# Performance work log

Measured on AMD Instinct MI355X. Metric: run time of the kernel, lower is better.

The kernel has to match this reference:

```python
import jax, jax.numpy as jnp
import numpy as np

N_ATOMS = 100000
N_BONDS = 200000
MAX_NB = 6
ATOM_FDIM = 133
BOND_FDIM = 147
HIDDEN = 512
N_MOLS = 8192
DEPTH = 5


def setup_inputs() -> dict:
    key = jax.random.key(0)
    ks = jax.random.split(key, 10)
    f_atoms = jax.random.normal(ks[0], (N_ATOMS, ATOM_FDIM), dtype=jnp.float32)
    f_bonds = jax.random.normal(ks[1], (N_BONDS, BOND_FDIM), dtype=jnp.float32)
    # fan-in scaled weights to keep activations stable through the depth loop
    W_i = jax.random.normal(ks[2], (BOND_FDIM, HIDDEN), dtype=jnp.float32) / np.sqrt(BOND_FDIM)
    W_h = jax.random.normal(ks[3], (HIDDEN, HIDDEN), dtype=jnp.float32) / np.sqrt(HIDDEN)
    W_o = jax.random.normal(ks[4], (ATOM_FDIM + HIDDEN, HIDDEN), dtype=jnp.float32) / np.sqrt(ATOM_FDIM + HIDDEN)
    b_o = jnp.zeros((HIDDEN,), dtype=jnp.float32)
    a2b = jax.random.randint(ks[5], (N_ATOMS, MAX_NB), 0, N_BONDS, dtype=jnp.int32)
    b2a = jax.random.randint(ks[6], (N_BONDS,), 0, N_ATOMS, dtype=jnp.int32)
    b2revb = jax.random.randint(ks[7], (N_BONDS,), 0, N_BONDS, dtype=jnp.int32)
    atom_to_mol = jnp.sort(jax.random.randint(ks[8], (N_ATOMS,), 0, N_MOLS, dtype=jnp.int32))
    return {"f_atoms": f_atoms, "f_bonds": f_bonds, "W_i": W_i, "W_h": W_h,
            "W_o": W_o, "b_o": b_o, "a2b": a2b, "b2a": b2a, "b2revb": b2revb,
            "atom_to_mol": atom_to_mol, "n_mols": N_MOLS}


def reference(f_atoms, f_bonds, W_i, W_h, W_o, b_o, a2b, b2a, b2revb, atom_to_mol, n_mols):
    # input = W_i(f_bonds); message = relu(input)
    inp = f_bonds @ W_i                      # [B, H]
    message = jax.nn.relu(inp)
    for _ in range(DEPTH - 1):
        nei_a_message = message[a2b]         # [A, MAX_NB, H] gather bond->atom
        a_message = nei_a_message.sum(axis=1)  # [A, H]
        message = a_message[b2a] - message[b2revb]  # [B, H]
        message = jax.nn.relu(inp + message @ W_h)  # dropout p=0 -> identity
    nei_a_message = message[a2b]             # [A, MAX_NB, H]
    a_message = nei_a_message.sum(axis=1)    # [A, H]
    a_input = jnp.concatenate([f_atoms, a_message], axis=1)  # [A, ATOM_FDIM+H]
    atom_hiddens = jax.nn.relu(a_input @ W_o + b_o)           # [A, H]
    # mean aggregation per molecule (a_scope -> segment ids)
    sums = jax.ops.segment_sum(atom_hiddens, atom_to_mol, num_segments=n_mols)
    counts = jax.ops.segment_sum(jnp.ones((atom_hiddens.shape[0],), dtype=atom_hiddens.dtype),
                                 atom_to_mol, num_segments=n_mols)
    mol_vecs = jnp.where(counts[:, None] > 0,
                         sums / jnp.maximum(counts, 1.0)[:, None],
                         jnp.zeros_like(sums))  # cached_zero_vector for empty mols
    return mol_vecs
```

## Files before the change

### kernel.cpp

```cpp
#include <hip/hip_runtime.h>
#include <hip/hip_bf16.h>
#include <cstdint>

#define A_N   100000
#define B_N   200000
#define MAXNB 6
#define AFD   133
#define BFD   147
#define HID   512
#define NMOL  8192

typedef __attribute__((ext_vector_type(8))) short bf16x8;
typedef __attribute__((ext_vector_type(4))) float f32x4;

__device__ __forceinline__ unsigned short f2b(float f) {
    unsigned u = __builtin_bit_cast(unsigned, f);
    u += 0x7fffu + ((u >> 16) & 1u);
    return (unsigned short)(u >> 16);
}
__device__ __forceinline__ float blo(unsigned u) { return __builtin_bit_cast(float, u << 16); }
__device__ __forceinline__ float bhi(unsigned u) { return __builtin_bit_cast(float, u & 0xffff0000u); }
__device__ __forceinline__ unsigned pack2f(float a, float b) {
    return (unsigned)f2b(a) | ((unsigned)f2b(b) << 16);
}
__device__ __forceinline__ void glds16(const void* g, void* l) {
    __builtin_amdgcn_global_load_lds((const __attribute__((address_space(1))) unsigned*)g,
                                     (__attribute__((address_space(3))) unsigned*)l, 16, 0, 0);
}

__global__ __launch_bounds__(256) void k_diag(float* __restrict__ out, int n, float val) {
    int i = blockIdx.x * 256 + threadIdx.x;
    if (i < n) out[i] = val;
}

__global__ __launch_bounds__(256) void k_weights(
    const float* __restrict__ Wi, const float* __restrict__ Wh, const float* __restrict__ Wo,
    unsigned short* __restrict__ WiT, unsigned short* __restrict__ WcatImg, unsigned short* __restrict__ WoT)
{
    int n = blockIdx.x, t = threadIdx.x;
    for (int k = t; k < 160; k += 256)
        WiT[(size_t)n * 160 + k] = (k < BFD) ? f2b(Wi[(size_t)k * HID + n]) : (unsigned short)0;
    for (int k = t; k < 672; k += 256) {
        unsigned short v;
        if (k < HID)             v = f2b(Wh[(size_t)k * HID + n]);
        else if (k < HID + BFD)  v = f2b(Wi[(size_t)(k - HID) * HID + n]);
        else                     v = 0;
        int row = n & 127;
        size_t tile = (size_t)(n >> 7) * 21 + (k >> 5);
        WcatImg[tile * 4096 + row * 32 + ((((k >> 3) & 3) ^ ((row >> 1) & 3)) << 3) + (k & 7)] = v;
    }
    for (int k = t; k < 672; k += 256) {
        unsigned short v;
        if (k < AFD)       v = f2b(Wo[(size_t)k * HID + n]);
        else if (k < 160)  v = 0;
        else               v = f2b(Wo[(size_t)(k - 27) * HID + n]);
        WoT[(size_t)n * 672 + k] = v;
    }
}

__global__ __launch_bounds__(256) void k_gemm_wi(
    const float* __restrict__ fb, const unsigned short* __restrict__ WiT,
    unsigned short* __restrict__ msg)
{
    __shared__ unsigned short As[128][32];
    __shared__ unsigned short Bs[128][32];
    const int orig = blockIdx.x;
    const int xcd = orig & 7, idx = orig >> 3;
    const int wg = (xcd < 4 ? xcd * 782 : 3128 + (xcd - 4) * 781) + idx;
    const int bm = wg >> 2, bn = wg & 3;
    const int row0 = bm * 128, col0 = bn * 128;

    const int tid = threadIdx.x, lane = tid & 63, wid = tid >> 6;
    const int wm = wid >> 1, wn = wid & 1;
    const int r0 = tid >> 2, c0 = tid & 3, r1 = 64 + r0;
    const int wsw = (c0 ^ ((r0 >> 1) & 3)) * 8;
    const int rsw = ((lane >> 4) ^ (((lane & 15) >> 1) & 3)) * 8;
    f32x4 acc[4][4] = {};

    const float* pf0 = fb + (size_t)min(row0 + r0, B_N - 1) * BFD;
    const float* pf1 = fb + (size_t)min(row0 + r1, B_N - 1) * BFD;
    const unsigned short* pb0 = WiT + (size_t)(col0 + r0) * 160;
    const unsigned short* pb1 = WiT + (size_t)(col0 + r1) * 160;

    float v0[8], v1[8];
    uint4 b0, b1;

#define LOADA(kt) do { int kb = (kt) * 32 + c0 * 8; \
        _Pragma("unroll") for (int i = 0; i < 8; i++) { int kg = kb + i; v0[i] = (kg < BFD) ? pf0[kg] : 0.f; } \
        _Pragma("unroll") for (int i = 0; i < 8; i++) { int kg = kb + i; v1[i] = (kg < BFD) ? pf1[kg] : 0.f; } } while (0)
#define LOADB(kt) do { int kb = (kt) * 32 + c0 * 8; \
        b0 = *(const uint4*)(pb0 + kb); b1 = *(const uint4*)(pb1 + kb); } while (0)

    LOADA(0); LOADB(0);
    for (int kt = 0; kt < 5; ++kt) {
        __syncthreads();
        uint4 q;
        q.x = pack2f(v0[0], v0[1]); q.y = pack2f(v0[2], v0[3]); q.z = pack2f(v0[4], v0[5]); q.w = pack2f(v0[6], v0[7]);
        *(uint4*)&As[r0][wsw] = q;
        q.x = pack2f(v1[0], v1[1]); q.y = pack2f(v1[2], v1[3]); q.z = pack2f(v1[4], v1[5]); q.w = pack2f(v1[6], v1[7]);
        *(uint4*)&As[r1][wsw] = q;
        *(uint4*)&Bs[r0][wsw] = b0;
        *(uint4*)&Bs[r1][wsw] = b1;
        __syncthreads();
        if (kt < 4) { LOADA(kt + 1); LOADB(kt + 1); }

        bf16x8 af[4], bfr[4];
#pragma unroll
        for (int m = 0; m < 4; m++) af[m] = *(const bf16x8*)&As[wm * 64 + m * 16 + (lane & 15)][rsw];
#pragma unroll
        for (int n = 0; n < 4; n++) bfr[n] = *(const bf16x8*)&Bs[wn * 64 + n * 16 + (lane & 15)][rsw];
#pragma unroll
        for (int m = 0; m < 4; m++)
#pragma unroll
            for (int n = 0; n < 4; n++)
                acc[m][n] = __builtin_amdgcn_mfma_f32_16x16x32_bf16(af[m], bfr[n], acc[m][n], 0, 0, 0);
    }
#undef LOADA
#undef LOADB

#pragma unroll
    for (int m = 0; m < 4; m++) {
        int rbase = row0 + wm * 64 + m * 16 + (lane >> 4) * 4;
#pragma unroll
        for (int n = 0; n < 4; n++) {
            int cg = col0 + wn * 64 + n * 16 + (lane & 15);
#pragma unroll
            for (int r = 0; r < 4; r++) {
                int rg = rbase + r;
                if (rg < B_N) {
                    float v = acc[m][n][r];
                    msg[(size_t)rg * HID + cg] = f2b(v > 0.f ? v : 0.f);
                }
            }
        }
    }
}

__global__ __launch_bounds__(256) void k_delta(
    const unsigned short* __restrict__ msg, const int* __restrict__ a2b,
    const int* __restrict__ b2a, const int* __restrict__ b2revb,
    unsigned short* __restrict__ D)
{
    int b = blockIdx.x * 4 + (threadIdx.x >> 6);
    if (b >= B_N) return;
    int lane = threadIdx.x & 63;
    const int atom = b2a[b];
    const int rev  = b2revb[b];
    const int* nb = a2b + (size_t)atom * MAXNB;
    float acc[8];
    {
        uint4 v = *(const uint4*)(msg + (size_t)rev * HID + lane * 8);
        acc[0] = -blo(v.x); acc[1] = -bhi(v.x);
        acc[2] = -blo(v.y); acc[3] = -bhi(v.y);
        acc[4] = -blo(v.z); acc[5] = -bhi(v.z);
        acc[6] = -blo(v.w); acc[7] = -bhi(v.w);
    }
#pragma unroll
    for (int k = 0; k < MAXNB; k++) {
        uint4 v = *(const uint4*)(msg + (size_t)nb[k] * HID + lane * 8);
        acc[0] += blo(v.x); acc[1] += bhi(v.x);
        acc[2] += blo(v.y); acc[3] += bhi(v.y);
        acc[4] += blo(v.z); acc[5] += bhi(v.z);
        acc[6] += blo(v.w); acc[7] += bhi(v.w);
    }
    uint4 q;
    q.x = pack2f(acc[0], acc[1]); q.y = pack2f(acc[2], acc[3]);
    q.z = pack2f(acc[4], acc[5]); q.w = pack2f(acc[6], acc[7]);
    *(uint4*)(D + (size_t)b * HID + lane * 8) = q;
}

__global__ __launch_bounds__(256) void k_gemm_wh(
    const unsigned short* __restrict__ D, const float* __restrict__ fb,
    const unsigned short* __restrict__ WcatImg,
    unsigned short* __restrict__ msg_out)
{
    __shared__ unsigned short As[128][32];
    __shared__ unsigned short Bs[2][4096];
    const int orig = blockIdx.x;
    const int xcd = orig & 7, idx = orig >> 3;
    const int wg = (xcd < 4 ? xcd * 782 : 3128 + (xcd - 4) * 781) + idx;
    const int bm = wg >> 2, bn = wg & 3;
    const int row0 = bm * 128;

    const int tid = threadIdx.x, lane = tid & 63, wid = tid >> 6;
    const int wm = wid >> 1, wn = wid & 1;
    const int r0 = tid >> 2, c0 = tid & 3, r1 = 64 + r0;
    const int wsw = (c0 ^ ((r0 >> 1) & 3)) * 8;
    const int rsw = ((lane >> 4) ^ (((lane & 15) >> 1) & 3)) * 8;
    f32x4 acc[4][4] = {};

    const int rg0 = min(row0 + r0, B_N - 1), rg1 = min(row0 + r1, B_N - 1);
    const unsigned short* pd0 = D + (size_t)rg0 * HID;
    const unsigned short* pd1 = D + (size_t)rg1 * HID;
    const float* pf0 = fb + (size_t)rg0 * BFD;
    const float* pf1 = fb + (size_t)rg1 * BFD;
    const char* img = (const char*)WcatImg + (size_t)bn * 21 * 8192;
    char* bsb = (char*)&Bs[0][0] + wid * 2048;

    uint4 a0, a1;
    float v0[8], v1[8];

#define GLDSB(kt, buf) do { \
        const char* s = img + (size_t)(kt) * 8192 + wid * 2048 + lane * 16; \
        char* d = bsb + (buf) * 8192; \
        glds16(s, d); \
        glds16(s + 1024, d + 1024); } while (0)
#define LOADA_D(kt) do { int kb = (kt) * 32 + c0 * 8; \
        a0 = *(const uint4*)(pd0 + kb); a1 = *(const uint4*)(pd1 + kb); } while (0)
#define LOADA_F(kt) do { int kb = (kt) * 32 - HID + c0 * 8; \
        _Pragma("unroll") for (int i = 0; i < 8; i++) { int kg = kb + i; v0[i] = (kg < BFD) ? pf0[kg] : 0.f; } \
        _Pragma("unroll") for (int i = 0; i < 8; i++) { int kg = kb + i; v1[i] = (kg < BFD) ? pf1[kg] : 0.f; } } while (0)

    GLDSB(0, 0);
    LOADA_D(0);
    for (int kt = 0; kt < 21; ++kt) {
        __syncthreads();
        if (kt < 16) {
            *(uint4*)&As[r0][wsw] = a0;
            *(uint4*)&As[r1][wsw] = a1;
        } else {
            uint4 q;
            q.x = pack2f(v0[0], v0[1]); q.y = pack2f(v0[2], v0[3]); q.z = pack2f(v0[4], v0[5]); q.w = pack2f(v0[6], v0[7]);
            *(uint4*)&As[r0][wsw] = q;
            q.x = pack2f(v1[0], v1[1]); q.y = pack2f(v1[2], v1[3]); q.z = pack2f(v1[4], v1[5]); q.w = pack2f(v1[6], v1[7]);
            *(uint4*)&As[r1][wsw] = q;
        }
        __syncthreads();
        if (kt < 20) {
            GLDSB(kt + 1, (kt + 1) & 1);
            if (kt + 1 < 16) LOADA_D(kt + 1); else LOADA_F(kt + 1);
        }
        bf16x8 af[4], bfr[4];
#pragma unroll
        for (int m = 0; m < 4; m++) af[m] = *(const bf16x8*)&As[wm * 64 + m * 16 + (lane & 15)][rsw];
#pragma unroll
        for (int n = 0; n < 4; n++) bfr[n] = *(const bf16x8*)&Bs[kt & 1][(wn * 64 + n * 16 + (lane & 15)) * 32 + rsw];
#pragma unroll
        for (int m = 0; m < 4; m++)
#pragma unroll
            for (int n = 0; n < 4; n++)
                acc[m][n] = __builtin_amdgcn_mfma_f32_16x16x32_bf16(af[m], bfr[n], acc[m][n], 0, 0, 0);
    }
#undef GLDSB
#undef LOADA_D
#undef LOADA_F

#pragma unroll
    for (int m = 0; m < 4; m++) {
        int rbase = row0 + wm * 64 + m * 16 + (lane >> 4) * 4;
#pragma unroll
        for (int n = 0; n < 4; n++) {
            int cg = bn * 128 + wn * 64 + n * 16 + (lane & 15);
#pragma unroll
            for (int r = 0; r < 4; r++) {
                int rg = rbase + r;
                if (rg < B_N) {
                    float v = acc[m][n][r];
                    msg_out[(size_t)rg * HID + cg] = f2b(v > 0.f ? v : 0.f);
                }
            }
        }
    }
}

__global__ __launch_bounds__(256) void k_gemm_wo(
    const float* __restrict__ fa, const unsigned short* __restrict__ amsg,
    const unsigned short* __restrict__ WoT, const float* __restrict__ bo,
    float* __restrict__ ah)
{
    __shared__ unsigned short As[128][32];
    __shared__ unsigned short Bs[128][32];
    const int orig = blockIdx.x;
    const int wg = (orig & 7) * 391 + (orig >> 3);
    const int bm = wg >> 2, bn = wg & 3;
    const int row0 = bm * 128, col0 = bn * 128;

    const int tid = threadIdx.x, lane = tid & 63, wid = tid >> 6;
    const int wm = wid >> 1, wn = wid & 1;
    const int r0 = tid >> 2, c0 = tid & 3, r1 = 64 + r0;
    const int wsw = (c0 ^ ((r0 >> 1) & 3)) * 8;
    const int rsw = ((lane >> 4) ^ (((lane & 15) >> 1) & 3)) * 8;
    f32x4 acc[4][4] = {};

    const int rg0 = min(row0 + r0, A_N - 1), rg1 = min(row0 + r1, A_N - 1);
    const float* pf0 = fa + (size_t)rg0 * AFD;
    const float* pf1 = fa + (size_t)rg1 * AFD;
    const unsigned short* pm0 = amsg + (size_t)rg0 * HID;
    const unsigned short* pm1 = amsg + (size_t)rg1 * HID;
    const unsigned short* pb0 = WoT + (size_t)(col0 + r0) * 672;
    const unsigned short* pb1 = WoT + (size_t)(col0 + r1) * 672;

    uint4 a0, a1, b0, b1;
    float v0[8], v1[8];

#define LOADA(kt) do { \
        if ((kt) < 5) { int kb = (kt) * 32 + c0 * 8; \
            _Pragma("unroll") for (int i = 0; i < 8; i++) { int kg = kb + i; v0[i] = (kg < AFD) ? pf0[kg] : 0.f; } \
            _Pragma("unroll") for (int i = 0; i < 8; i++) { int kg = kb + i; v1[i] = (kg < AFD) ? pf1[kg] : 0.f; } \
        } else { int kb = (kt) * 32 - 160 + c0 * 8; \
            a0 = *(const uint4*)(pm0 + kb); a1 = *(const uint4*)(pm1 + kb); } } while (0)
#define LOADB(kt) do { int kb = (kt) * 32 + c0 * 8; \
        b0 = *(const uint4*)(pb0 + kb); b1 = *(const uint4*)(pb1 + kb); } while (0)

    LOADA(0); LOADB(0);
    for (int kt = 0; kt < 21; ++kt) {
        __syncthreads();
        if (kt < 5) {
            uint4 q;
            q.x = pack2f(v0[0], v0[1]); q.y = pack2f(v0[2], v0[3]); q.z = pack2f(v0[4], v0[5]); q.w = pack2f(v0[6], v0[7]);
            *(uint4*)&As[r0][wsw] = q;
            q.x = pack2f(v1[0], v1[1]); q.y = pack2f(v1[2], v1[3]); q.z = pack2f(v1[4], v1[5]); q.w = pack2f(v1[6], v1[7]);
            *(uint4*)&As[r1][wsw] = q;
        } else {
            *(uint4*)&As[r0][wsw] = a0;
            *(uint4*)&As[r1][wsw] = a1;
        }
        *(uint4*)&Bs[r0][wsw] = b0;
        *(uint4*)&Bs[r1][wsw] = b1;
        __syncthreads();
        if (kt < 20) { LOADA(kt + 1); LOADB(kt + 1); }

        bf16x8 af[4], bfr[4];
#pragma unroll
        for (int m = 0; m < 4; m++) af[m] = *(const bf16x8*)&As[wm * 64 + m * 16 + (lane & 15)][rsw];
#pragma unroll
        for (int n = 0; n < 4; n++) bfr[n] = *(const bf16x8*)&Bs[wn * 64 + n * 16 + (lane & 15)][rsw];
#pragma unroll
        for (int m = 0; m < 4; m++)
#pragma unroll
            for (int n = 0; n < 4; n++)
                acc[m][n] = __builtin_amdgcn_mfma_f32_16x16x32_bf16(af[m], bfr[n], acc[m][n], 0, 0, 0);
    }
#undef LOADA
#undef LOADB

#pragma unroll
    for (int m = 0; m < 4; m++) {
        int rbase = row0 + wm * 64 + m * 16 + (lane >> 4) * 4;
#pragma unroll
        for (int n = 0; n < 4; n++) {
            int cg = col0 + wn * 64 + n * 16 + (lane & 15);
            float bias = bo[cg];
#pragma unroll
            for (int r = 0; r < 4; r++) {
                int rg = rbase + r;
                if (rg < A_N) {
                    float v = acc[m][n][r] + bias;
                    ah[(size_t)rg * HID + cg] = v > 0.f ? v : 0.f;
                }
            }
        }
    }
}

__global__ __launch_bounds__(256) void k_gather(
    const unsigned short* __restrict__ msg, const int* __restrict__ a2b,
    unsigned short* __restrict__ amsg)
{
    int g = blockIdx.x * 4 + (threadIdx.x >> 6);
    if (g >= A_N) return;
    int lane = threadIdx.x & 63;
    const int* nb = a2b + (size_t)g * MAXNB;
    float acc[8] = {};
#pragma unroll
    for (int k = 0; k < MAXNB; k++) {
        uint4 v = *(const uint4*)(msg + (size_t)nb[k] * HID + lane * 8);
        acc[0] += blo(v.x); acc[1] += bhi(v.x);
        acc[2] += blo(v.y); acc[3] += bhi(v.y);
        acc[4] += blo(v.z); acc[5] += bhi(v.z);
        acc[6] += blo(v.w); acc[7] += bhi(v.w);
    }
    uint4 q;
    q.x = pack2f(acc[0], acc[1]); q.y = pack2f(acc[2], acc[3]);
    q.z = pack2f(acc[4], acc[5]); q.w = pack2f(acc[6], acc[7]);
    *(uint4*)(amsg + (size_t)g * HID + lane * 8) = q;
}

__global__ __launch_bounds__(256) void k_segmean(
    const float* __restrict__ ah, const int* __restrict__ a2m, float* __restrict__ out)
{
    int mol = blockIdx.x, t = threadIdx.x;
    int lo, hi;
    { int l = 0, r = A_N; while (l < r) { int m = (l + r) >> 1; if (a2m[m] < mol) l = m + 1; else r = m; } lo = l; }
    { int l = lo, r = A_N; while (l < r) { int m = (l + r) >> 1; if (a2m[m] < mol + 1) l = m + 1; else r = m; } hi = l; }
    float s0 = 0.f, s1 = 0.f;
    for (int a = lo; a < hi; a++) {
        s0 += ah[(size_t)a * HID + t];
        s1 += ah[(size_t)a * HID + 256 + t];
    }
    int c = hi - lo;
    float inv = c > 0 ? 1.0f / (float)c : 0.f;
    out[(size_t)mol * HID + t] = s0 * inv;
    out[(size_t)mol * HID + 256 + t] = s1 * inv;
}

extern "C" void kernel_launch(void* const* d_in, const int* in_sizes, int n_in,
                              void* d_out, int out_size, void* d_ws, size_t ws_size,
                              hipStream_t stream)
{
    const float* f_atoms = (const float*)d_in[0];
    const float* f_bonds = (const float*)d_in[1];
    const float* W_i     = (const float*)d_in[2];
    const float* W_h     = (const float*)d_in[3];
    const float* W_o     = (const float*)d_in[4];
    const float* b_o     = (const float*)d_in[5];
    const int*   a2b     = (const int*)d_in[6];
    const int*   b2a     = (const int*)d_in[7];
    const int*   b2revb  = (const int*)d_in[8];
    const int*   a2m     = (const int*)d_in[9];

    const size_t OFF_MSG  = 0;
    const size_t OFF_D    = 204800000;
    const size_t OFF_WIT  = 409600000;
    const size_t OFF_WCAT = 409763840;
    const size_t OFF_WOT  = 410451968;
    const size_t REQUIRED = 411140096;

    if (ws_size < REQUIRED) {
        float val = -(10000.0f + (float)(ws_size >> 20));
        k_diag<<<dim3((out_size + 255) / 256), dim3(256), 0, stream>>>((float*)d_out, out_size, val);
        return;
    }

    char* w = (char*)d_ws;
    unsigned short* msg   = (unsigned short*)(w + OFF_MSG);
    unsigned short* D     = (unsigned short*)(w + OFF_D);
    unsigned short* amsg  = (unsigned short*)(w + OFF_D);
    unsigned short* WiT   = (unsigned short*)(w + OFF_WIT);
    unsigned short* Wcat  = (unsigned short*)(w + OFF_WCAT);
    unsigned short* WoT   = (unsigned short*)(w + OFF_WOT);
    float* ah             = (float*)(w + OFF_MSG);

    k_weights<<<dim3(512), dim3(256), 0, stream>>>(W_i, W_h, W_o, WiT, Wcat, WoT);
    k_gemm_wi<<<dim3(6252), dim3(256), 0, stream>>>(f_bonds, WiT, msg);
    for (int it = 0; it < 4; ++it) {
        k_delta<<<dim3(50000), dim3(256), 0, stream>>>(msg, a2b, b2a, b2revb, D);
        k_gemm_wh<<<dim3(6252), dim3(256), 0, stream>>>(D, f_bonds, Wcat, msg);
    }
    k_gather<<<dim3(25000), dim3(256), 0, stream>>>(msg, a2b, amsg);
    k_gemm_wo<<<dim3(3128), dim3(256), 0, stream>>>(f_atoms, amsg, WoT, b_o, ah);
    k_segmean<<<dim3(NMOL), dim3(256), 0, stream>>>(ah, a2m, (float*)d_out);
}
```

Baseline: 2.448 ms.

## Load GEMM A/B tiles directly into double-buffered LDS and drop a barrier

Both bf16 GEMM kernels (W_h message update and W_o readout) now fetch their bf16 A and B tiles with direct global-to-LDS loads into double-buffered shared memory. This replaces staging them through registers and then storing them to LDS. As a result, the second __syncthreads per k-step is only needed for the fp32 feature tiles that still go through registers. The kernels also get a launch-bounds occupancy hint of 4 blocks. The aim is to cut register pressure, VGPR-to-LDS traffic and barrier stalls, at the cost of twice the shared memory and possibly lower occupancy.

```diff
diff --git a/kernel.cpp b/kernel.cpp
--- a/kernel.cpp
+++ b/kernel.cpp
@@ -169,12 +169,12 @@
     *(uint4*)(D + (size_t)b * HID + lane * 8) = q;
 }
 
-__global__ __launch_bounds__(256) void k_gemm_wh(
+__global__ __launch_bounds__(256, 4) void k_gemm_wh(
     const unsigned short* __restrict__ D, const float* __restrict__ fb,
     const unsigned short* __restrict__ WcatImg,
     unsigned short* __restrict__ msg_out)
 {
-    __shared__ unsigned short As[128][32];
+    __shared__ unsigned short As[2][128][32];
     __shared__ unsigned short Bs[2][4096];
     const int orig = blockIdx.x;
     const int xcd = orig & 7, idx = orig >> 3;
@@ -189,61 +189,60 @@
     const int rsw = ((lane >> 4) ^ (((lane & 15) >> 1) & 3)) * 8;
     f32x4 acc[4][4] = {};
 
+    const int arow1 = wid * 32 + (lane >> 2);
+    const int arow2 = arow1 + 16;
+    const int achk = lane & 3;
+    const unsigned short* srcA1 = D + (size_t)min(row0 + arow1, B_N - 1) * HID + ((achk ^ ((arow1 >> 1) & 3)) << 3);
+    const unsigned short* srcA2 = D + (size_t)min(row0 + arow2, B_N - 1) * HID + ((achk ^ ((arow2 >> 1) & 3)) << 3);
+    const char* srcB = (const char*)WcatImg + (size_t)bn * 21 * 8192 + wid * 2048 + lane * 16;
+
     const int rg0 = min(row0 + r0, B_N - 1), rg1 = min(row0 + r1, B_N - 1);
-    const unsigned short* pd0 = D + (size_t)rg0 * HID;
-    const unsigned short* pd1 = D + (size_t)rg1 * HID;
     const float* pf0 = fb + (size_t)rg0 * BFD;
     const float* pf1 = fb + (size_t)rg1 * BFD;
-    const char* img = (const char*)WcatImg + (size_t)bn * 21 * 8192;
-    char* bsb = (char*)&Bs[0][0] + wid * 2048;
-
-    uint4 a0, a1;
     float v0[8], v1[8];
 
-#define GLDSB(kt, buf) do { \
-        const char* s = img + (size_t)(kt) * 8192 + wid * 2048 + lane * 16; \
-        char* d = bsb + (buf) * 8192; \
-        glds16(s, d); \
-        glds16(s + 1024, d + 1024); } while (0)
-#define LOADA_D(kt) do { int kb = (kt) * 32 + c0 * 8; \
-        a0 = *(const uint4*)(pd0 + kb); a1 = *(const uint4*)(pd1 + kb); } while (0)
-#define LOADA_F(kt) do { int kb = (kt) * 32 - HID + c0 * 8; \
-        _Pragma("unroll") for (int i = 0; i < 8; i++) { int kg = kb + i; v0[i] = (kg < BFD) ? pf0[kg] : 0.f; } \
-        _Pragma("unroll") for (int i = 0; i < 8; i++) { int kg = kb + i; v1[i] = (kg < BFD) ? pf1[kg] : 0.f; } } while (0)
-
-    GLDSB(0, 0);
-    LOADA_D(0);
+    glds16(srcA1, &As[0][wid * 32][0]);
+    glds16(srcA2, &As[0][wid * 32 + 16][0]);
+    glds16(srcB, &Bs[0][wid * 1024]);
+    glds16(srcB + 1024, &Bs[0][wid * 1024 + 512]);
+
     for (int kt = 0; kt < 21; ++kt) {
+        const int cur = kt & 1, nxt = cur ^ 1;
         __syncthreads();
-        if (kt < 16) {
-            *(uint4*)&As[r0][wsw] = a0;
-            *(uint4*)&As[r1][wsw] = a1;
-        } else {
+        if (kt >= 16) {
             uint4 q;
             q.x = pack2f(v0[0], v0[1]); q.y = pack2f(v0[2], v0[3]); q.z = pack2f(v0[4], v0[5]); q.w = pack2f(v0[6], v0[7]);
-            *(uint4*)&As[r0][wsw] = q;
+            *(uint4*)&As[cur][r0][wsw] = q;
             q.x = pack2f(v1[0], v1[1]); q.y = pack2f(v1[2], v1[3]); q.z = pack2f(v1[4], v1[5]); q.w = pack2f(v1[6], v1[7]);
-            *(uint4*)&As[r1][wsw] = q;
-        }
-        __syncthreads();
+            *(uint4*)&As[cur][r1][wsw] = q;
+            __syncthreads();
+        }
         if (kt < 20) {
-            GLDSB(kt + 1, (kt + 1) & 1);
-            if (kt + 1 < 16) LOADA_D(kt + 1); else LOADA_F(kt + 1);
+            if (kt + 1 < 16) {
+                glds16(srcA1 + (kt + 1) * 32, &As[nxt][wid * 32][0]);
+                glds16(srcA2 + (kt + 1) * 32, &As[nxt][wid * 32 + 16][0]);
+            }
+            glds16(srcB + (size_t)(kt + 1) * 8192, &Bs[nxt][wid * 1024]);
+            glds16(srcB + (size_t)(kt + 1) * 8192 + 1024, &Bs[nxt][wid * 1024 + 512]);
+        }
+        if (kt >= 15 && kt < 20) {
+            int kb = (kt + 1) * 32 - HID + c0 * 8;
+#pragma unroll
+            for (int i = 0; i < 8; i++) { int kg = kb + i; v0[i] = (kg < BFD) ? pf0[kg] : 0.f; }
+#pragma unroll
+            for (int i = 0; i < 8; i++) { int kg = kb + i; v1[i] = (kg < BFD) ? pf1[kg] : 0.f; }
         }
         bf16x8 af[4], bfr[4];
 #pragma unroll
-        for (int m = 0; m < 4; m++) af[m] = *(const bf16x8*)&As[wm * 64 + m * 16 + (lane & 15)][rsw];
-#pragma unroll
-        for (int n = 0; n < 4; n++) bfr[n] = *(const bf16x8*)&Bs[kt & 1][(wn * 64 + n * 16 + (lane & 15)) * 32 + rsw];
+        for (int m = 0; m < 4; m++) af[m] = *(const bf16x8*)&As[cur][wm * 64 + m * 16 + (lane & 15)][rsw];
+#pragma unroll
+        for (int n = 0; n < 4; n++) bfr[n] = *(const bf16x8*)&Bs[cur][(wn * 64 + n * 16 + (lane & 15)) * 32 + rsw];
 #pragma unroll
         for (int m = 0; m < 4; m++)
 #pragma unroll
             for (int n = 0; n < 4; n++)
                 acc[m][n] = __builtin_amdgcn_mfma_f32_16x16x32_bf16(af[m], bfr[n], acc[m][n], 0, 0, 0);
     }
-#undef GLDSB
-#undef LOADA_D
-#undef LOADA_F
 
 #pragma unroll
     for (int m = 0; m < 4; m++) {
@@ -263,13 +262,13 @@
     }
 }
 
-__global__ __launch_bounds__(256) void k_gemm_wo(
+__global__ __launch_bounds__(256, 4) void k_gemm_wo(
     const float* __restrict__ fa, const unsigned short* __restrict__ amsg,
     const unsigned short* __restrict__ WoT, const float* __restrict__ bo,
     float* __restrict__ ah)
 {
-    __shared__ unsigned short As[128][32];
-    __shared__ unsigned short Bs[128][32];
+    __shared__ unsigned short As[2][128][32];
+    __shared__ unsigned short Bs[2][128][32];
     const int orig = blockIdx.x;
     const int wg = (orig & 7) * 391 + (orig >> 3);
     const int bm = wg >> 2, bn = wg & 3;
@@ -282,57 +281,68 @@
     const int rsw = ((lane >> 4) ^ (((lane & 15) >> 1) & 3)) * 8;
     f32x4 acc[4][4] = {};
 
+    const int grow1 = wid * 32 + (lane >> 2);
+    const int grow2 = grow1 + 16;
+    const int gchk = lane & 3;
+    const int asw1 = (gchk ^ ((grow1 >> 1) & 3)) << 3;
+    const int asw2 = (gchk ^ ((grow2 >> 1) & 3)) << 3;
+    const unsigned short* srcA1 = amsg + (size_t)min(row0 + grow1, A_N - 1) * HID + asw1 - 160;
+    const unsigned short* srcA2 = amsg + (size_t)min(row0 + grow2, A_N - 1) * HID + asw2 - 160;
+    const unsigned short* srcB1 = WoT + (size_t)(col0 + grow1) * 672 + asw1;
+    const unsigned short* srcB2 = WoT + (size_t)(col0 + grow2) * 672 + asw2;
+
     const int rg0 = min(row0 + r0, A_N - 1), rg1 = min(row0 + r1, A_N - 1);
     const float* pf0 = fa + (size_t)rg0 * AFD;
     const float* pf1 = fa + (size_t)rg1 * AFD;
-    const unsigned short* pm0 = amsg + (size_t)rg0 * HID;
-    const unsigned short* pm1 = amsg + (size_t)rg1 * HID;
-    const unsigned short* pb0 = WoT + (size_t)(col0 + r0) * 672;
-    const unsigned short* pb1 = WoT + (size_t)(col0 + r1) * 672;
-
-    uint4 a0, a1, b0, b1;
     float v0[8], v1[8];
 
-#define LOADA(kt) do { \
-        if ((kt) < 5) { int kb = (kt) * 32 + c0 * 8; \
-            _Pragma("unroll") for (int i = 0; i < 8; i++) { int kg = kb + i; v0[i] = (kg < AFD) ? pf0[kg] : 0.f; } \
-            _Pragma("unroll") for (int i = 0; i < 8; i++) { int kg = kb + i; v1[i] = (kg < AFD) ? pf1[kg] : 0.f; } \
-        } else { int kb = (kt) * 32 - 160 + c0 * 8; \
-            a0 = *(const uint4*)(pm0 + kb); a1 = *(const uint4*)(pm1 + kb); } } while (0)
-#define LOADB(kt) do { int kb = (kt) * 32 + c0 * 8; \
-        b0 = *(const uint4*)(pb0 + kb); b1 = *(const uint4*)(pb1 + kb); } while (0)
-
-    LOADA(0); LOADB(0);
+    {
+        int kb = c0 * 8;
+#pragma unroll
+        for (int i = 0; i < 8; i++) { int kg = kb + i; v0[i] = (kg < AFD) ? pf0[kg] : 0.f; }
+#pragma unroll
+        for (int i = 0; i < 8; i++) { int kg = kb + i; v1[i] = (kg < AFD) ? pf1[kg] : 0.f; }
+    }
+    glds16(srcB1, &Bs[0][wid * 32][0]);
+    glds16(srcB2, &Bs[0][wid * 32 + 16][0]);
+
     for (int kt = 0; kt < 21; ++kt) {
+        const int cur = kt & 1, nxt = cur ^ 1;
         __syncthreads();
         if (kt < 5) {
             uint4 q;
             q.x = pack2f(v0[0], v0[1]); q.y = pack2f(v0[2], v0[3]); q.z = pack2f(v0[4], v0[5]); q.w = pack2f(v0[6], v0[7]);
-            *(uint4*)&As[r0][wsw] = q;
+            *(uint4*)&As[cur][r0][wsw] = q;
             q.x = pack2f(v1[0], v1[1]); q.y = pack2f(v1[2], v1[3]); q.z = pack2f(v1[4], v1[5]); q.w = pack2f(v1[6], v1[7]);
-            *(uint4*)&As[r1][wsw] = q;
-        } else {
-            *(uint4*)&As[r0][wsw] = a0;
-            *(uint4*)&As[r1][wsw] = a1;
-        }
-        *(uint4*)&Bs[r0][wsw] = b0;
-        *(uint4*)&Bs[r1][wsw] = b1;
-        __syncthreads();
-        if (kt < 20) { LOADA(kt + 1); LOADB(kt + 1); }
-
+            *(uint4*)&As[cur][r1][wsw] = q;
+            __syncthreads();
+        }
+        if (kt < 20) {
+            if (kt + 1 >= 5) {
+                glds16(srcA1 + (kt + 1) * 32, &As[nxt][wid * 32][0]);
+                glds16(srcA2 + (kt + 1) * 32, &As[nxt][wid * 32 + 16][0]);
+            }
+            glds16(srcB1 + (kt + 1) * 32, &Bs[nxt][wid * 32][0]);
+            glds16(srcB2 + (kt + 1) * 32, &Bs[nxt][wid * 32 + 16][0]);
+        }
+        if (kt < 4) {
+            int kb = (kt + 1) * 32 + c0 * 8;
+#pragma unroll
+            for (int i = 0; i < 8; i++) { int kg = kb + i; v0[i] = (kg < AFD) ? pf0[kg] : 0.f; }
+#pragma unroll
+            for (int i = 0; i < 8; i++) { int kg = kb + i; v1[i] = (kg < AFD) ? pf1[kg] : 0.f; }
+        }
         bf16x8 af[4], bfr[4];
 #pragma unroll
-        for (int m = 0; m < 4; m++) af[m] = *(const bf16x8*)&As[wm * 64 + m * 16 + (lane & 15)][rsw];
-#pragma unroll
-        for (int n = 0; n < 4; n++) bfr[n] = *(const bf16x8*)&Bs[wn * 64 + n * 16 + (lane & 15)][rsw];
+        for (int m = 0; m < 4; m++) af[m] = *(const bf16x8*)&As[cur][wm * 64 + m * 16 + (lane & 15)][rsw];
+#pragma unroll
+        for (int n = 0; n < 4; n++) bfr[n] = *(const bf16x8*)&Bs[cur][wn * 64 + n * 16 + (lane & 15)][rsw];
 #pragma unroll
         for (int m = 0; m < 4; m++)
 #pragma unroll
             for (int n = 0; n < 4; n++)
                 acc[m][n] = __builtin_amdgcn_mfma_f32_16x16x32_bf16(af[m], bfr[n], acc[m][n], 0, 0, 0);
     }
-#undef LOADA
-#undef LOADB
 
 #pragma unroll
     for (int m = 0; m < 4; m++) {
```

New measurement: 2.384 ms. 1.03x faster.

## Triple-buffer GEMM tiles with direct-to-LDS loads and issue gathers up front

Applied to the files above, without the earlier changes.

The Wh and Wo GEMMs now stage both A and B tiles through three LDS buffers filled by global_load_lds, with explicit vmcnt waits and barriers. This replaces register staging and double buffering so loads for two tiles ahead overlap the MFMA work. The Wo weights are repacked into the same swizzled tile image, and the K order is changed to put the message part first and the atom features last. The gather and delta kernels now issue all neighbour loads before summing, to expose memory-level parallelism. The cost is more LDS per block, hand-written waitcnt logic that must stay exact, and an occupancy hint of 3 blocks per CU.

```diff
diff --git a/kernel.cpp b/kernel.cpp
--- a/kernel.cpp
+++ b/kernel.cpp
@@ -28,6 +28,11 @@
                                      (__attribute__((address_space(3))) unsigned*)l, 16, 0, 0);
 }
 
+#define WAIT4 asm volatile("s_waitcnt vmcnt(4)" ::: "memory")
+#define WAIT2 asm volatile("s_waitcnt vmcnt(2)" ::: "memory")
+#define SB0   __builtin_amdgcn_sched_barrier(0)
+#define BAR   __builtin_amdgcn_s_barrier()
+
 __global__ __launch_bounds__(256) void k_diag(float* __restrict__ out, int n, float val) {
     int i = blockIdx.x * 256 + threadIdx.x;
     if (i < n) out[i] = val;
@@ -35,9 +40,10 @@
 
 __global__ __launch_bounds__(256) void k_weights(
     const float* __restrict__ Wi, const float* __restrict__ Wh, const float* __restrict__ Wo,
-    unsigned short* __restrict__ WiT, unsigned short* __restrict__ WcatImg, unsigned short* __restrict__ WoT)
+    unsigned short* __restrict__ WiT, unsigned short* __restrict__ WcatImg, unsigned short* __restrict__ WoImg)
 {
     int n = blockIdx.x, t = threadIdx.x;
+    int row = n & 127;
     for (int k = t; k < 160; k += 256)
         WiT[(size_t)n * 160 + k] = (k < BFD) ? f2b(Wi[(size_t)k * HID + n]) : (unsigned short)0;
     for (int k = t; k < 672; k += 256) {
@@ -45,16 +51,16 @@
         if (k < HID)             v = f2b(Wh[(size_t)k * HID + n]);
         else if (k < HID + BFD)  v = f2b(Wi[(size_t)(k - HID) * HID + n]);
         else                     v = 0;
-        int row = n & 127;
         size_t tile = (size_t)(n >> 7) * 21 + (k >> 5);
         WcatImg[tile * 4096 + row * 32 + ((((k >> 3) & 3) ^ ((row >> 1) & 3)) << 3) + (k & 7)] = v;
     }
     for (int k = t; k < 672; k += 256) {
         unsigned short v;
-        if (k < AFD)       v = f2b(Wo[(size_t)k * HID + n]);
-        else if (k < 160)  v = 0;
-        else               v = f2b(Wo[(size_t)(k - 27) * HID + n]);
-        WoT[(size_t)n * 672 + k] = v;
+        if (k < 512)       v = f2b(Wo[(size_t)(k + 133) * HID + n]);
+        else if (k < 645)  v = f2b(Wo[(size_t)(k - 512) * HID + n]);
+        else               v = 0;
+        size_t tile = (size_t)(n >> 7) * 21 + (k >> 5);
+        WoImg[tile * 4096 + row * 32 + ((((k >> 3) & 3) ^ ((row >> 1) & 3)) << 3) + (k & 7)] = v;
     }
 }
 
@@ -147,35 +153,35 @@
     const int atom = b2a[b];
     const int rev  = b2revb[b];
     const int* nb = a2b + (size_t)atom * MAXNB;
+    uint4 g0 = *(const uint4*)(msg + (size_t)nb[0] * HID + lane * 8);
+    uint4 g1 = *(const uint4*)(msg + (size_t)nb[1] * HID + lane * 8);
+    uint4 g2 = *(const uint4*)(msg + (size_t)nb[2] * HID + lane * 8);
+    uint4 g3 = *(const uint4*)(msg + (size_t)nb[3] * HID + lane * 8);
+    uint4 g4 = *(const uint4*)(msg + (size_t)nb[4] * HID + lane * 8);
+    uint4 g5 = *(const uint4*)(msg + (size_t)nb[5] * HID + lane * 8);
+    uint4 gr = *(const uint4*)(msg + (size_t)rev * HID + lane * 8);
     float acc[8];
-    {
-        uint4 v = *(const uint4*)(msg + (size_t)rev * HID + lane * 8);
-        acc[0] = -blo(v.x); acc[1] = -bhi(v.x);
-        acc[2] = -blo(v.y); acc[3] = -bhi(v.y);
-        acc[4] = -blo(v.z); acc[5] = -bhi(v.z);
-        acc[6] = -blo(v.w); acc[7] = -bhi(v.w);
-    }
-#pragma unroll
-    for (int k = 0; k < MAXNB; k++) {
-        uint4 v = *(const uint4*)(msg + (size_t)nb[k] * HID + lane * 8);
-        acc[0] += blo(v.x); acc[1] += bhi(v.x);
-        acc[2] += blo(v.y); acc[3] += bhi(v.y);
-        acc[4] += blo(v.z); acc[5] += bhi(v.z);
-        acc[6] += blo(v.w); acc[7] += bhi(v.w);
-    }
+    acc[0] = blo(g0.x) + blo(g1.x) + blo(g2.x) + blo(g3.x) + blo(g4.x) + blo(g5.x) - blo(gr.x);
+    acc[1] = bhi(g0.x) + bhi(g1.x) + bhi(g2.x) + bhi(g3.x) + bhi(g4.x) + bhi(g5.x) - bhi(gr.x);
+    acc[2] = blo(g0.y) + blo(g1.y) + blo(g2.y) + blo(g3.y) + blo(g4.y) + blo(g5.y) - blo(gr.y);
+    acc[3] = bhi(g0.y) + bhi(g1.y) + bhi(g2.y) + bhi(g3.y) + bhi(g4.y) + bhi(g5.y) - bhi(gr.y);
+    acc[4] = blo(g0.z) + blo(g1.z) + blo(g2.z) + blo(g3.z) + blo(g4.z) + blo(g5.z) - blo(gr.z);
+    acc[5] = bhi(g0.z) + bhi(g1.z) + bhi(g2.z) + bhi(g3.z) + bhi(g4.z) + bhi(g5.z) - bhi(gr.z);
+    acc[6] = blo(g0.w) + blo(g1.w) + blo(g2.w) + blo(g3.w) + blo(g4.w) + blo(g5.w) - blo(gr.w);
+    acc[7] = bhi(g0.w) + bhi(g1.w) + bhi(g2.w) + bhi(g3.w) + bhi(g4.w) + bhi(g5.w) - bhi(gr.w);
     uint4 q;
     q.x = pack2f(acc[0], acc[1]); q.y = pack2f(acc[2], acc[3]);
     q.z = pack2f(acc[4], acc[5]); q.w = pack2f(acc[6], acc[7]);
     *(uint4*)(D + (size_t)b * HID + lane * 8) = q;
 }
 
-__global__ __launch_bounds__(256) void k_gemm_wh(
+__global__ __launch_bounds__(256, 3) void k_gemm_wh(
     const unsigned short* __restrict__ D, const float* __restrict__ fb,
     const unsigned short* __restrict__ WcatImg,
     unsigned short* __restrict__ msg_out)
 {
-    __shared__ unsigned short As[128][32];
-    __shared__ unsigned short Bs[2][4096];
+    __shared__ unsigned short As[3][128][32];
+    __shared__ unsigned short Bs[3][4096];
     const int orig = blockIdx.x;
     const int xcd = orig & 7, idx = orig >> 3;
     const int wg = (xcd < 4 ? xcd * 782 : 3128 + (xcd - 4) * 781) + idx;
@@ -189,61 +195,76 @@
     const int rsw = ((lane >> 4) ^ (((lane & 15) >> 1) & 3)) * 8;
     f32x4 acc[4][4] = {};
 
+    const int arow1 = wid * 32 + (lane >> 2);
+    const int arow2 = arow1 + 16;
+    const int achk = lane & 3;
+    const unsigned short* srcA1 = D + (size_t)min(row0 + arow1, B_N - 1) * HID + ((achk ^ ((arow1 >> 1) & 3)) << 3);
+    const unsigned short* srcA2 = D + (size_t)min(row0 + arow2, B_N - 1) * HID + ((achk ^ ((arow2 >> 1) & 3)) << 3);
+    const char* srcB = (const char*)WcatImg + (size_t)bn * 21 * 8192 + wid * 2048 + lane * 16;
+
     const int rg0 = min(row0 + r0, B_N - 1), rg1 = min(row0 + r1, B_N - 1);
-    const unsigned short* pd0 = D + (size_t)rg0 * HID;
-    const unsigned short* pd1 = D + (size_t)rg1 * HID;
     const float* pf0 = fb + (size_t)rg0 * BFD;
     const float* pf1 = fb + (size_t)rg1 * BFD;
-    const char* img = (const char*)WcatImg + (size_t)bn * 21 * 8192;
-    char* bsb = (char*)&Bs[0][0] + wid * 2048;
-
-    uint4 a0, a1;
     float v0[8], v1[8];
 
-#define GLDSB(kt, buf) do { \
-        const char* s = img + (size_t)(kt) * 8192 + wid * 2048 + lane * 16; \
-        char* d = bsb + (buf) * 8192; \
-        glds16(s, d); \
-        glds16(s + 1024, d + 1024); } while (0)
-#define LOADA_D(kt) do { int kb = (kt) * 32 + c0 * 8; \
-        a0 = *(const uint4*)(pd0 + kb); a1 = *(const uint4*)(pd1 + kb); } while (0)
-#define LOADA_F(kt) do { int kb = (kt) * 32 - HID + c0 * 8; \
+#define COMPUTE(b) do { \
+        bf16x8 af[4], bfr[4]; \
+        _Pragma("unroll") \
+        for (int m = 0; m < 4; m++) af[m] = *(const bf16x8*)&As[b][wm * 64 + m * 16 + (lane & 15)][rsw]; \
+        _Pragma("unroll") \
+        for (int n = 0; n < 4; n++) bfr[n] = *(const bf16x8*)&Bs[b][(wn * 64 + n * 16 + (lane & 15)) * 32 + rsw]; \
+        _Pragma("unroll") \
+        for (int m = 0; m < 4; m++) \
+        _Pragma("unroll") \
+        for (int n = 0; n < 4; n++) \
+            acc[m][n] = __builtin_amdgcn_mfma_f32_16x16x32_bf16(af[m], bfr[n], acc[m][n], 0, 0, 0); \
+    } while (0)
+#define GLDS_STEP(kt, buf) do { \
+        glds16(srcA1 + (kt) * 32, &As[buf][wid * 32][0]); \
+        glds16(srcA2 + (kt) * 32, &As[buf][wid * 32 + 16][0]); \
+        glds16(srcB + (size_t)(kt) * 8192, &Bs[buf][wid * 1024]); \
+        glds16(srcB + (size_t)(kt) * 8192 + 1024, &Bs[buf][wid * 1024 + 512]); } while (0)
+#define LOADFB(kt) do { int kb = (kt) * 32 - HID + c0 * 8; \
         _Pragma("unroll") for (int i = 0; i < 8; i++) { int kg = kb + i; v0[i] = (kg < BFD) ? pf0[kg] : 0.f; } \
         _Pragma("unroll") for (int i = 0; i < 8; i++) { int kg = kb + i; v1[i] = (kg < BFD) ? pf1[kg] : 0.f; } } while (0)
 
-    GLDSB(0, 0);
-    LOADA_D(0);
-    for (int kt = 0; kt < 21; ++kt) {
-        __syncthreads();
-        if (kt < 16) {
-            *(uint4*)&As[r0][wsw] = a0;
-            *(uint4*)&As[r1][wsw] = a1;
-        } else {
-            uint4 q;
-            q.x = pack2f(v0[0], v0[1]); q.y = pack2f(v0[2], v0[3]); q.z = pack2f(v0[4], v0[5]); q.w = pack2f(v0[6], v0[7]);
-            *(uint4*)&As[r0][wsw] = q;
-            q.x = pack2f(v1[0], v1[1]); q.y = pack2f(v1[2], v1[3]); q.z = pack2f(v1[4], v1[5]); q.w = pack2f(v1[6], v1[7]);
-            *(uint4*)&As[r1][wsw] = q;
+    LOADFB(16);
+    GLDS_STEP(0, 0);
+    GLDS_STEP(1, 1);
+
+#pragma unroll
+    for (int kt = 0; kt < 14; ++kt) {
+        WAIT4; SB0; BAR; SB0;
+        GLDS_STEP(kt + 2, (kt + 2) % 3);
+        SB0;
+        COMPUTE(kt % 3);
+    }
+    WAIT4; SB0; BAR; SB0;
+    glds16(srcB + (size_t)16 * 8192, &Bs[1][wid * 1024]);
+    glds16(srcB + (size_t)16 * 8192 + 1024, &Bs[1][wid * 1024 + 512]);
+    SB0;
+    COMPUTE(2);
+    WAIT2; SB0; BAR; SB0;
+    COMPUTE(0);
+
+    for (int kt = 16; kt < 21; ++kt) {
+        const int cb = kt % 3;
+        __syncthreads();
+        uint4 q;
+        q.x = pack2f(v0[0], v0[1]); q.y = pack2f(v0[2], v0[3]); q.z = pack2f(v0[4], v0[5]); q.w = pack2f(v0[6], v0[7]);
+        *(uint4*)&As[cb][r0][wsw] = q;
+        q.x = pack2f(v1[0], v1[1]); q.y = pack2f(v1[2], v1[3]); q.z = pack2f(v1[4], v1[5]); q.w = pack2f(v1[6], v1[7]);
+        *(uint4*)&As[cb][r1][wsw] = q;
+        __syncthreads();
+        if (kt < 20) {
+            glds16(srcB + (size_t)(kt + 1) * 8192, &Bs[(kt + 1) % 3][wid * 1024]);
+            glds16(srcB + (size_t)(kt + 1) * 8192 + 1024, &Bs[(kt + 1) % 3][wid * 1024 + 512]);
+            LOADFB(kt + 1);
         }
-        __syncthreads();
-        if (kt < 20) {
-            GLDSB(kt + 1, (kt + 1) & 1);
-            if (kt + 1 < 16) LOADA_D(kt + 1); else LOADA_F(kt + 1);
-        }
-        bf16x8 af[4], bfr[4];
-#pragma unroll
-        for (int m = 0; m < 4; m++) af[m] = *(const bf16x8*)&As[wm * 64 + m * 16 + (lane & 15)][rsw];
-#pragma unroll
-        for (int n = 0; n < 4; n++) bfr[n] = *(const bf16x8*)&Bs[kt & 1][(wn * 64 + n * 16 + (lane & 15)) * 32 + rsw];
-#pragma unroll
-        for (int m = 0; m < 4; m++)
-#pragma unroll
-            for (int n = 0; n < 4; n++)
-                acc[m][n] = __builtin_amdgcn_mfma_f32_16x16x32_bf16(af[m], bfr[n], acc[m][n], 0, 0, 0);
-    }
-#undef GLDSB
-#undef LOADA_D
-#undef LOADA_F
+        COMPUTE(cb);
+    }
+#undef GLDS_STEP
+#undef LOADFB
 
 #pragma unroll
     for (int m = 0; m < 4; m++) {
@@ -261,19 +282,20 @@
             }
         }
     }
-}
-
-__global__ __launch_bounds__(256) void k_gemm_wo(
+#undef COMPUTE
+}
+
+__global__ __launch_bounds__(256, 3) void k_gemm_wo(
     const float* __restrict__ fa, const unsigned short* __restrict__ amsg,
-    const unsigned short* __restrict__ WoT, const float* __restrict__ bo,
+    const unsigned short* __restrict__ WoImg, const float* __restrict__ bo,
     float* __restrict__ ah)
 {
-    __shared__ unsigned short As[128][32];
-    __shared__ unsigned short Bs[128][32];
+    __shared__ unsigned short As[3][128][32];
+    __shared__ unsigned short Bs[3][4096];
     const int orig = blockIdx.x;
     const int wg = (orig & 7) * 391 + (orig >> 3);
     const int bm = wg >> 2, bn = wg & 3;
-    const int row0 = bm * 128, col0 = bn * 128;
+    const int row0 = bm * 128;
 
     const int tid = threadIdx.x, lane = tid & 63, wid = tid >> 6;
     const int wm = wid >> 1, wn = wid & 1;
@@ -282,64 +304,83 @@
     const int rsw = ((lane >> 4) ^ (((lane & 15) >> 1) & 3)) * 8;
     f32x4 acc[4][4] = {};
 
+    const int arow1 = wid * 32 + (lane >> 2);
+    const int arow2 = arow1 + 16;
+    const int achk = lane & 3;
+    const unsigned short* srcA1 = amsg + (size_t)min(row0 + arow1, A_N - 1) * HID + ((achk ^ ((arow1 >> 1) & 3)) << 3);
+    const unsigned short* srcA2 = amsg + (size_t)min(row0 + arow2, A_N - 1) * HID + ((achk ^ ((arow2 >> 1) & 3)) << 3);
+    const char* srcB = (const char*)WoImg + (size_t)bn * 21 * 8192 + wid * 2048 + lane * 16;
+
     const int rg0 = min(row0 + r0, A_N - 1), rg1 = min(row0 + r1, A_N - 1);
     const float* pf0 = fa + (size_t)rg0 * AFD;
     const float* pf1 = fa + (size_t)rg1 * AFD;
-    const unsigned short* pm0 = amsg + (size_t)rg0 * HID;
-    const unsigned short* pm1 = amsg + (size_t)rg1 * HID;
-    const unsigned short* pb0 = WoT + (size_t)(col0 + r0) * 672;
-    const unsigned short* pb1 = WoT + (size_t)(col0 + r1) * 672;
-
-    uint4 a0, a1, b0, b1;
     float v0[8], v1[8];
 
-#define LOADA(kt) do { \
-        if ((kt) < 5) { int kb = (kt) * 32 + c0 * 8; \
-            _Pragma("unroll") for (int i = 0; i < 8; i++) { int kg = kb + i; v0[i] = (kg < AFD) ? pf0[kg] : 0.f; } \
-            _Pragma("unroll") for (int i = 0; i < 8; i++) { int kg = kb + i; v1[i] = (kg < AFD) ? pf1[kg] : 0.f; } \
-        } else { int kb = (kt) * 32 - 160 + c0 * 8; \
-            a0 = *(const uint4*)(pm0 + kb); a1 = *(const uint4*)(pm1 + kb); } } while (0)
-#define LOADB(kt) do { int kb = (kt) * 32 + c0 * 8; \
-        b0 = *(const uint4*)(pb0 + kb); b1 = *(const uint4*)(pb1 + kb); } while (0)
-
-    LOADA(0); LOADB(0);
-    for (int kt = 0; kt < 21; ++kt) {
-        __syncthreads();
-        if (kt < 5) {
-            uint4 q;
-            q.x = pack2f(v0[0], v0[1]); q.y = pack2f(v0[2], v0[3]); q.z = pack2f(v0[4], v0[5]); q.w = pack2f(v0[6], v0[7]);
-            *(uint4*)&As[r0][wsw] = q;
-            q.x = pack2f(v1[0], v1[1]); q.y = pack2f(v1[2], v1[3]); q.z = pack2f(v1[4], v1[5]); q.w = pack2f(v1[6], v1[7]);
-            *(uint4*)&As[r1][wsw] = q;
-        } else {
-            *(uint4*)&As[r0][wsw] = a0;
-            *(uint4*)&As[r1][wsw] = a1;
+#define COMPUTE(b) do { \
+        bf16x8 af[4], bfr[4]; \
+        _Pragma("unroll") \
+        for (int m = 0; m < 4; m++) af[m] = *(const bf16x8*)&As[b][wm * 64 + m * 16 + (lane & 15)][rsw]; \
+        _Pragma("unroll") \
+        for (int n = 0; n < 4; n++) bfr[n] = *(const bf16x8*)&Bs[b][(wn * 64 + n * 16 + (lane & 15)) * 32 + rsw]; \
+        _Pragma("unroll") \
+        for (int m = 0; m < 4; m++) \
+        _Pragma("unroll") \
+        for (int n = 0; n < 4; n++) \
+            acc[m][n] = __builtin_amdgcn_mfma_f32_16x16x32_bf16(af[m], bfr[n], acc[m][n], 0, 0, 0); \
+    } while (0)
+#define GLDS_STEP(kt, buf) do { \
+        glds16(srcA1 + (kt) * 32, &As[buf][wid * 32][0]); \
+        glds16(srcA2 + (kt) * 32, &As[buf][wid * 32 + 16][0]); \
+        glds16(srcB + (size_t)(kt) * 8192, &Bs[buf][wid * 1024]); \
+        glds16(srcB + (size_t)(kt) * 8192 + 1024, &Bs[buf][wid * 1024 + 512]); } while (0)
+#define LOADFA(kt) do { int kb = (kt) * 32 - HID + c0 * 8; \
+        _Pragma("unroll") for (int i = 0; i < 8; i++) { int kg = kb + i; v0[i] = (kg < AFD) ? pf0[kg] : 0.f; } \
+        _Pragma("unroll") for (int i = 0; i < 8; i++) { int kg = kb + i; v1[i] = (kg < AFD) ? pf1[kg] : 0.f; } } while (0)
+
+    LOADFA(16);
+    GLDS_STEP(0, 0);
+    GLDS_STEP(1, 1);
+
+#pragma unroll
+    for (int kt = 0; kt < 14; ++kt) {
+        WAIT4; SB0; BAR; SB0;
+        GLDS_STEP(kt + 2, (kt + 2) % 3);
+        SB0;
+        COMPUTE(kt % 3);
+    }
+    WAIT4; SB0; BAR; SB0;
+    glds16(srcB + (size_t)16 * 8192, &Bs[1][wid * 1024]);
+    glds16(srcB + (size_t)16 * 8192 + 1024, &Bs[1][wid * 1024 + 512]);
+    SB0;
+    COMPUTE(2);
+    WAIT2; SB0; BAR; SB0;
+    COMPUTE(0);
+
+    for (int kt = 16; kt < 21; ++kt) {
+        const int cb = kt % 3;
+        __syncthreads();
+        uint4 q;
+        q.x = pack2f(v0[0], v0[1]); q.y = pack2f(v0[2], v0[3]); q.z = pack2f(v0[4], v0[5]); q.w = pack2f(v0[6], v0[7]);
+        *(uint4*)&As[cb][r0][wsw] = q;
+        q.x = pack2f(v1[0], v1[1]); q.y = pack2f(v1[2], v1[3]); q.z = pack2f(v1[4], v1[5]); q.w = pack2f(v1[6], v1[7]);
+        *(uint4*)&As[cb][r1][wsw] = q;
+        __syncthreads();
+        if (kt < 20) {
+            glds16(srcB + (size_t)(kt + 1) * 8192, &Bs[(kt + 1) % 3][wid * 1024]);
+            glds16(srcB + (size_t)(kt + 1) * 8192 + 1024, &Bs[(kt + 1) % 3][wid * 1024 + 512]);
+            LOADFA(kt + 1);
         }
-        *(uint4*)&Bs[r0][wsw] = b0;
-        *(uint4*)&Bs[r1][wsw] = b1;
-        __syncthreads();
-        if (kt < 20) { LOADA(kt + 1); LOADB(kt + 1); }
-
-        bf16x8 af[4], bfr[4];
-#pragma unroll
-        for (int m = 0; m < 4; m++) af[m] = *(const bf16x8*)&As[wm * 64 + m * 16 + (lane & 15)][rsw];
-#pragma unroll
-        for (int n = 0; n < 4; n++) bfr[n] = *(const bf16x8*)&Bs[wn * 64 + n * 16 + (lane & 15)][rsw];
-#pragma unroll
-        for (int m = 0; m < 4; m++)
-#pragma unroll
-            for (int n = 0; n < 4; n++)
-                acc[m][n] = __builtin_amdgcn_mfma_f32_16x16x32_bf16(af[m], bfr[n], acc[m][n], 0, 0, 0);
-    }
-#undef LOADA
-#undef LOADB
+        COMPUTE(cb);
+    }
+#undef GLDS_STEP
+#undef LOADFA
 
 #pragma unroll
     for (int m = 0; m < 4; m++) {
         int rbase = row0 + wm * 64 + m * 16 + (lane >> 4) * 4;
 #pragma unroll
         for (int n = 0; n < 4; n++) {
-            int cg = col0 + wn * 64 + n * 16 + (lane & 15);
+            int cg = bn * 128 + wn * 64 + n * 16 + (lane & 15);
             float bias = bo[cg];
 #pragma unroll
             for (int r = 0; r < 4; r++) {
@@ -351,6 +392,7 @@
             }
         }
     }
+#undef COMPUTE
 }
 
 __global__ __launch_bounds__(256) void k_gather(
@@ -361,15 +403,21 @@
     if (g >= A_N) return;
     int lane = threadIdx.x & 63;
     const int* nb = a2b + (size_t)g * MAXNB;
-    float acc[8] = {};
-#pragma unroll
-    for (int k = 0; k < MAXNB; k++) {
-        uint4 v = *(const uint4*)(msg + (size_t)nb[k] * HID + lane * 8);
-        acc[0] += blo(v.x); acc[1] += bhi(v.x);
-        acc[2] += blo(v.y); acc[3] += bhi(v.y);
-        acc[4] += blo(v.z); acc[5] += bhi(v.z);
-        acc[6] += blo(v.w); acc[7] += bhi(v.w);
-    }
+    uint4 g0 = *(const uint4*)(msg + (size_t)nb[0] * HID + lane * 8);
+    uint4 g1 = *(const uint4*)(msg + (size_t)nb[1] * HID + lane * 8);
+    uint4 g2 = *(const uint4*)(msg + (size_t)nb[2] * HID + lane * 8);
+    uint4 g3 = *(const uint4*)(msg + (size_t)nb[3] * HID + lane * 8);
+    uint4 g4 = *(const uint4*)(msg + (size_t)nb[4] * HID + lane * 8);
+    uint4 g5 = *(const uint4*)(msg + (size_t)nb[5] * HID + lane * 8);
+    float acc[8];
+    acc[0] = blo(g0.x) + blo(g1.x) + blo(g2.x) + blo(g3.x) + blo(g4.x) + blo(g5.x);
+    acc[1] = bhi(g0.x) + bhi(g1.x) + bhi(g2.x) + bhi(g3.x) + bhi(g4.x) + bhi(g5.x);
+    acc[2] = blo(g0.y) + blo(g1.y) + blo(g2.y) + blo(g3.y) + blo(g4.y) + blo(g5.y);
+    acc[3] = bhi(g0.y) + bhi(g1.y) + bhi(g2.y) + bhi(g3.y) + bhi(g4.y) + bhi(g5.y);
+    acc[4] = blo(g0.z) + blo(g1.z) + blo(g2.z) + blo(g3.z) + blo(g4.z) + blo(g5.z);
+    acc[5] = bhi(g0.z) + bhi(g1.z) + bhi(g2.z) + bhi(g3.z) + bhi(g4.z) + bhi(g5.z);
+    acc[6] = blo(g0.w) + blo(g1.w) + blo(g2.w) + blo(g3.w) + blo(g4.w) + blo(g5.w);
+    acc[7] = bhi(g0.w) + bhi(g1.w) + bhi(g2.w) + bhi(g3.w) + bhi(g4.w) + bhi(g5.w);
     uint4 q;
     q.x = pack2f(acc[0], acc[1]); q.y = pack2f(acc[2], acc[3]);
     q.z = pack2f(acc[4], acc[5]); q.w = pack2f(acc[6], acc[7]);
@@ -428,16 +476,16 @@
     unsigned short* amsg  = (unsigned short*)(w + OFF_D);
     unsigned short* WiT   = (unsigned short*)(w + OFF_WIT);
     unsigned short* Wcat  = (unsigned short*)(w + OFF_WCAT);
-    unsigned short* WoT   = (unsigned short*)(w + OFF_WOT);
+    unsigned short* WoImg = (unsigned short*)(w + OFF_WOT);
     float* ah             = (float*)(w + OFF_MSG);
 
-    k_weights<<<dim3(512), dim3(256), 0, stream>>>(W_i, W_h, W_o, WiT, Wcat, WoT);
+    k_weights<<<dim3(512), dim3(256), 0, stream>>>(W_i, W_h, W_o, WiT, Wcat, WoImg);
     k_gemm_wi<<<dim3(6252), dim3(256), 0, stream>>>(f_bonds, WiT, msg);
     for (int it = 0; it < 4; ++it) {
         k_delta<<<dim3(50000), dim3(256), 0, stream>>>(msg, a2b, b2a, b2revb, D);
         k_gemm_wh<<<dim3(6252), dim3(256), 0, stream>>>(D, f_bonds, Wcat, msg);
     }
     k_gather<<<dim3(25000), dim3(256), 0, stream>>>(msg, a2b, amsg);
-    k_gemm_wo<<<dim3(3128), dim3(256), 0, stream>>>(f_atoms, amsg, WoT, b_o, ah);
+    k_gemm_wo<<<dim3(3128), dim3(256), 0, stream>>>(f_atoms, amsg, WoImg, b_o, ah);
     k_segmean<<<dim3(NMOL), dim3(256), 0, stream>>>(ah, a2m, (float*)d_out);
 }
```

Measured after the change: 3.064 ms. 1.25x slower.
